# Optimization experiments

Measured on AMD Instinct MI355X. Metric: run time of the kernel, lower is better.

## Reference

```python
import jax, jax.numpy as jnp
import numpy as np
from math import ceil

B, N, C_IN, H, EDIM = 64, 512, 128, 128, 5
EPG = 16 * N          # edges per graph
E = B * EPG           # 524288 edges total
K1 = ceil(0.5 * N)    # 256 clusters after pool 1
K2 = ceil(0.5 * K1)   # 128 clusters after pool 2
EPS = 1e-15


def dense_mincut_pool(x, adj, s, mask=None):
    # x: [B,n,F], adj: [B,n,n], s: [B,n,k]
    s = jax.nn.softmax(s, axis=-1)
    if mask is not None:
        m = mask[..., None].astype(x.dtype)
        x = x * m
        s = s * m
    out = jnp.einsum('bnk,bnf->bkf', s, x)
    out_adj = jnp.einsum('bnk,bnm,bml->bkl', s, adj, s)
    mincut_num = jnp.trace(out_adj, axis1=-2, axis2=-1)
    d_flat = adj.sum(-1)                                   # degrees [B,n]
    mincut_den = jnp.trace(jnp.einsum('bnk,bn,bnl->bkl', s, d_flat, s), axis1=-2, axis2=-1)
    mincut_loss = jnp.mean(-(mincut_num / mincut_den))
    k = s.shape[-1]
    ss = jnp.einsum('bnk,bnl->bkl', s, s)
    ss_norm = jnp.linalg.norm(ss, axis=(-1, -2), keepdims=True)
    i_s = jnp.eye(k, dtype=x.dtype)
    ortho_loss = jnp.mean(jnp.linalg.norm(ss / ss_norm - i_s / np.sqrt(k), axis=(-1, -2)))
    out_adj = out_adj * (1.0 - i_s)                        # zero diagonal
    d = jnp.sqrt(out_adj.sum(-1))[..., None] + EPS
    out_adj = out_adj / d / jnp.swapaxes(d, -1, -2)
    return out, out_adj, mincut_loss, ortho_loss


def setup_inputs() -> dict:
    key = jax.random.key(0)
    ks = iter(jax.random.split(key, 40))
    NT = B * N
    x = jax.random.normal(next(ks), (NT, C_IN), jnp.float32)
    # within-graph random edges; nodes are sorted by graph (batch = repeat)
    offs = jnp.repeat(jnp.arange(B, dtype=jnp.int32) * N, EPG)
    src = jax.random.randint(next(ks), (E,), 0, N, jnp.int32) + offs
    dst = jax.random.randint(next(ks), (E,), 0, N, jnp.int32) + offs
    edge_index = jnp.stack([src, dst])
    edge_attr = jax.random.normal(next(ks), (E, EDIM), jnp.float32)
    batch = jnp.repeat(jnp.arange(B, dtype=jnp.int32), N)

    def W(shape):
        return jax.random.normal(next(ks), shape, jnp.float32) * 0.05

    inp = dict(x=x, edge_index=edge_index, edge_attr=edge_attr, batch=batch,
               bn_gamma=jnp.ones((C_IN,), jnp.float32), bn_beta=jnp.zeros((C_IN,), jnp.float32),
               Wq=W((C_IN, H)), bq=W((H,)), Wk=W((C_IN, H)), bk=W((H,)),
               Wv=W((C_IN, H)), bv=W((H,)), We=W((EDIM, H)),
               Wskip=W((C_IN, H)), bskip=W((H,)),
               W_mlp1=W((H, K1)), b_mlp1=W((K1,)),
               W2_rel=W((H, H)), b2_rel=W((H,)), W2_root=W((H, H)),
               W_mlp2=W((H, K2)), b_mlp2=W((K2,)),
               W3_rel=W((H, H)), b3_rel=W((H,)), W3_root=W((H, H)),
               W_lin1=W((H, H)), b_lin1=W((H,)),
               W_ro=W((H, 1)), b_ro=W((1,)))
    return inp


def reference(x, edge_index, edge_attr, batch, bn_gamma, bn_beta,
              Wq, bq, Wk, bk, Wv, bv, We, Wskip, bskip,
              W_mlp1, b_mlp1, W2_rel, b2_rel, W2_root,
              W_mlp2, b_mlp2, W3_rel, b3_rel, W3_root,
              W_lin1, b_lin1, W_ro, b_ro):
    NT = x.shape[0]
    # BatchNorm1d (training-mode batch statistics, biased var, eps=1e-5)
    mu = x.mean(0)
    var = x.var(0)
    xh = (x - mu) / jnp.sqrt(var + 1e-5) * bn_gamma + bn_beta

    # TransformerConv (heads=1, concat=True, root_weight=True, edge_dim=5)
    src, dst = edge_index[0], edge_index[1]
    q = xh @ Wq + bq
    k_ = xh @ Wk + bk
    v = xh @ Wv + bv
    e = edge_attr @ We                       # lin_edge has no bias
    kj = k_[src] + e
    vj = v[src] + e
    logits = (q[dst] * kj).sum(-1) / np.sqrt(H)
    m = jax.ops.segment_max(logits, dst, num_segments=NT)
    a = jnp.exp(logits - m[dst])
    denom = jax.ops.segment_sum(a, dst, num_segments=NT)
    alpha = a / denom[dst]
    agg = jax.ops.segment_sum(alpha[:, None] * vj, dst, num_segments=NT)
    h = jax.nn.relu(agg + xh @ Wskip + bskip)

    # to_dense_batch: equal-size graphs sorted by batch -> reshape
    xd = h.reshape(B, N, H)
    mask = jnp.ones((B, N), bool)
    # to_dense_adj: scatter-add edge indicators (duplicates accumulate)
    adj = jnp.zeros((B, N, N), jnp.float32).at[batch[src], src % N, dst % N].add(1.0)

    s = xd @ W_mlp1 + b_mlp1
    xd, adj, mc1, o1 = dense_mincut_pool(xd, adj, s, mask)
    # DenseGraphConv: lin_rel(adj @ x) + lin_root(x)
    xd = jax.nn.relu((adj @ xd) @ W2_rel + b2_rel + xd @ W2_root)
    s = xd @ W_mlp2 + b_mlp2
    xd, adj, mc2, o2 = dense_mincut_pool(xd, adj, s)
    xd = (adj @ xd) @ W3_rel + b3_rel + xd @ W3_root
    g = xd.mean(1)
    g = jax.nn.relu(g @ W_lin1 + b_lin1)
    return jax.nn.sigmoid(g @ W_ro + b_ro).squeeze(-1)   # [B]
```

## Files before the change

### kernel.cpp

```cpp
#include <hip/hip_runtime.h>
#include <math.h>

#define BGRAPH 64
#define NNODE  512
#define NTOT   32768
#define CIN    128
#define HDIM   128
#define EDIM_  5
#define EDGES  524288
#define K1C    256
#define K2C    128

using f32x4 = __attribute__((ext_vector_type(4))) float;
using s16x8 = __attribute__((ext_vector_type(8))) short;

__device__ __forceinline__ short f2bf(float f) {
    union { float f; unsigned u; } v; v.f = f;
    unsigned r = v.u + 0x7fffu + ((v.u >> 16) & 1u);
    return (short)(r >> 16);
}
__device__ __forceinline__ float bf2f(short s) {
    union { unsigned u; float f; } v; v.u = ((unsigned)(unsigned short)s) << 16;
    return v.f;
}

__global__ __launch_bounds__(256) void bn_stats_kernel(const float* __restrict__ x,
                                                       float* __restrict__ psum,
                                                       float* __restrict__ psq) {
    int tid = threadIdx.x, bid = blockIdx.x;
    long idx0 = (long)bid * 256 + tid;
    float4 s = {0.f, 0.f, 0.f, 0.f}, q = {0.f, 0.f, 0.f, 0.f};
#pragma unroll
    for (int it = 0; it < 16; ++it) {
        float4 v = *(const float4*)(x + (idx0 + (long)it * 65536) * 4);
        s.x += v.x; s.y += v.y; s.z += v.z; s.w += v.w;
        q.x += v.x * v.x; q.y += v.y * v.y; q.z += v.z * v.z; q.w += v.w * v.w;
    }
    __shared__ float ss[128], sq[128];
    if (tid < 128) { ss[tid] = 0.f; sq[tid] = 0.f; }
    __syncthreads();
    int c0 = (tid & 31) * 4;
    atomicAdd(&ss[c0 + 0], s.x); atomicAdd(&ss[c0 + 1], s.y);
    atomicAdd(&ss[c0 + 2], s.z); atomicAdd(&ss[c0 + 3], s.w);
    atomicAdd(&sq[c0 + 0], q.x); atomicAdd(&sq[c0 + 1], q.y);
    atomicAdd(&sq[c0 + 2], q.z); atomicAdd(&sq[c0 + 3], q.w);
    __syncthreads();
    if (tid < 128) {
        psum[bid * 128 + tid] = ss[tid];
        psq[bid * 128 + tid]  = sq[tid];
    }
}

__global__ __launch_bounds__(128) void bn_finalize_kernel(const float* __restrict__ psum,
                                                          const float* __restrict__ psq,
                                                          const float* __restrict__ gamma,
                                                          const float* __restrict__ beta,
                                                          float* __restrict__ scale,
                                                          float* __restrict__ shift) {
    int c = threadIdx.x;
    float s = 0.f, q = 0.f;
    for (int b = 0; b < 256; ++b) { s += psum[b * 128 + c]; q += psq[b * 128 + c]; }
    float mu  = s / (float)NTOT;
    float var = q / (float)NTOT - mu * mu;
    float rstd = rsqrtf(var + 1e-5f);
    float sc = gamma[c] * rstd;
    scale[c] = sc;
    shift[c] = beta[c] - mu * sc;
}

__global__ __launch_bounds__(256) void pack_hist_kernel(const float* __restrict__ Wq, const float* __restrict__ Wk,
                                                        const float* __restrict__ Wv, const float* __restrict__ Ws,
                                                        const float* __restrict__ bq, const float* __restrict__ bk,
                                                        const float* __restrict__ bv, const float* __restrict__ bs,
                                                        float* __restrict__ W4, float* __restrict__ bias4,
                                                        const int* __restrict__ ei,
                                                        int* __restrict__ deg_src,
                                                        int* __restrict__ deg_dst) {
    int bid = blockIdx.x;
    if (bid < 256) {
        int i = bid * 256 + threadIdx.x;
        if (i < 128 * 512) {
            int k = i / 512, j = i % 512;
            float v;
            if (j < 128)      v = Wq[k * 128 + j];
            else if (j < 256) v = Wk[k * 128 + (j - 128)];
            else if (j < 384) v = Wv[k * 128 + (j - 256)];
            else              v = Ws[k * 128 + (j - 384)];
            W4[i] = v;
        }
        if (i < 512) {
            float v;
            if (i < 128)      v = bq[i];
            else if (i < 256) v = bk[i - 128];
            else if (i < 384) v = bv[i - 256];
            else              v = bs[i - 384];
            bias4[i] = v;
        }
    } else {
        int e = (bid - 256) * 256 + threadIdx.x;
        if (e < EDGES) {
            atomicAdd(&deg_src[ei[e]], 1);
            atomicAdd(&deg_dst[ei[EDGES + e]], 1);
        }
    }
}

__global__ __launch_bounds__(1024) void scan2_kernel(const int* __restrict__ deg_src,
                                                     int* __restrict__ rp_src, int* __restrict__ cur_src,
                                                     const int* __restrict__ deg_dst,
                                                     int* __restrict__ rp_dst, int* __restrict__ cur_dst) {
    const int* deg = blockIdx.x ? deg_dst : deg_src;
    int* rowptr    = blockIdx.x ? rp_dst  : rp_src;
    int* cursor    = blockIdx.x ? cur_dst : cur_src;
    __shared__ int part[1024];
    int tid = threadIdx.x;
    int base = tid * 32;
    int s = 0;
    for (int i = 0; i < 32; ++i) s += deg[base + i];
    part[tid] = s;
    __syncthreads();
    for (int off = 1; off < 1024; off <<= 1) {
        int v = part[tid];
        int add = (tid >= off) ? part[tid - off] : 0;
        __syncthreads();
        part[tid] = v + add;
        __syncthreads();
    }
    int run = (tid == 0) ? 0 : part[tid - 1];
    for (int i = 0; i < 32; ++i) {
        rowptr[base + i] = run;
        cursor[base + i] = run;
        run += deg[base + i];
    }
}

__global__ __launch_bounds__(256) void scatter_kernel(const int* __restrict__ ei,
                                                      int* __restrict__ cur_src, int* __restrict__ cur_dst,
                                                      int* __restrict__ eid_src, int* __restrict__ eid_dst) {
    int e = blockIdx.x * 256 + threadIdx.x;
    if (e < EDGES) {
        int s = ei[e], d = ei[EDGES + e];
        eid_src[atomicAdd(&cur_src[s], 1)] = e;
        eid_dst[atomicAdd(&cur_dst[d], 1)] = e;
    }
}

template <int TILE, bool TRANS_A, bool AFFINE, bool ANORM, bool RELU, bool DUAL,
          bool OBF16, bool AU8, bool BBF16, bool ATRBF16, bool ABF16>
__global__ __launch_bounds__(256) void mgemm(const void* __restrict__ Av,
                                             const void* __restrict__ Bv,
                                             const void* __restrict__ A2v,
                                             const void* __restrict__ B2v,
                                             int Ksplit,
                                             const float* __restrict__ bias,
                                             void* __restrict__ Cv,
                                             const float* __restrict__ scale,
                                             const float* __restrict__ shift,
                                             int M, int Nc, int K,
                                             int lda, int ldb, int ldc,
                                             long sA, long sB, long sC) {
    __shared__ __align__(16) short As[TILE * 40];
    __shared__ __align__(16) short Bs[TILE * 40];
    constexpr int ASZ = AU8 ? 1 : ((ATRBF16 || ABF16) ? 2 : 4);
    constexpr int BSZ = BBF16 ? 2 : 4;
    const char* Abase = (const char*)Av + (long)blockIdx.z * sA * ASZ;
    const char* Bbase = (const char*)Bv + (long)blockIdx.z * sB * BSZ;
    float* C = (float*)Cv + (OBF16 ? 0 : (long)blockIdx.z * sC);
    short* Cs = (short*)Cv + (OBF16 ? (long)blockIdx.z * sC : 0);
    const int m0 = blockIdx.y * TILE, n0 = blockIdx.x * TILE;
    const int tid = threadIdx.x;
    const int lane16 = tid & 15;
    const int quad = (tid & 63) >> 4;
    const int wrow = (tid >> 6) >> 1, wcol = (tid >> 6) & 1;
    constexpr int WT = TILE / 32;

    f32x4 acc[WT][WT] = {};

    for (int k0 = 0; k0 < K; k0 += 32) {
        const char* Au = Abase; const char* Bu = Bbase; int ku = k0;
        if (DUAL && k0 >= Ksplit) { Au = (const char*)A2v; Bu = (const char*)B2v; ku = k0 - Ksplit; }

        if (!TRANS_A) {
#pragma unroll
            for (int p = 0; p < TILE / 32; ++p) {
                int idx = tid + p * 256;
                int row = idx >> 3, c4 = idx & 7;
                short4 o;
                if (AU8) {
                    unsigned u = *(const unsigned*)((const unsigned char*)Au +
                                                    (long)(m0 + row) * lda + ku + c4 * 4);
                    o = make_short4(f2bf((float)(u & 255u)), f2bf((float)((u >> 8) & 255u)),
                                    f2bf((float)((u >> 16) & 255u)), f2bf((float)((u >> 24) & 255u)));
                } else if (ABF16) {
                    o = *(const short4*)((const short*)Au + (long)(m0 + row) * lda + ku + c4 * 4);
                } else {
                    float4 v = *(const float4*)((const float*)Au + (long)(m0 + row) * lda + ku + c4 * 4);
                    if (AFFINE) {
                        int k = ku + c4 * 4;
                        v.x = v.x * scale[k] + shift[k];
                        v.y = v.y * scale[k + 1] + shift[k + 1];
                        v.z = v.z * scale[k + 2] + shift[k + 2];
                        v.w = v.w * scale[k + 3] + shift[k + 3];
                    }
                    if (ANORM) {
                        int k = ku + c4 * 4;
                        int grow = m0 + row;
                        const float* dv = scale + (long)blockIdx.z * lda;
                        float dr = dv[grow];
                        v.x = (grow == k + 0) ? 0.f : v.x * dr * dv[k + 0];
                        v.y = (grow == k + 1) ? 0.f : v.y * dr * dv[k + 1];
                        v.z = (grow == k + 2) ? 0.f : v.z * dr * dv[k + 2];
                        v.w = (grow == k + 3) ? 0.f : v.w * dr * dv[k + 3];
                    }
                    o = make_short4(f2bf(v.x), f2bf(v.y), f2bf(v.z), f2bf(v.w));
                }
                *(short4*)&As[row * 40 + c4 * 4] = o;
            }
        } else {
            if (TILE == 128 || tid < 128) {
                int c4 = tid >> 3, g = tid & 7;
                short* d = &As[(c4 * 4) * 40 + g * 4];
                if (ATRBF16) {
                    const short* src = (const short*)Au + (long)(ku + g * 4) * lda + m0 + c4 * 4;
                    short4 r0 = *(const short4*)(src);
                    short4 r1 = *(const short4*)(src + lda);
                    short4 r2 = *(const short4*)(src + 2 * lda);
                    short4 r3 = *(const short4*)(src + 3 * lda);
                    *(short4*)(d + 0 * 40) = make_short4(r0.x, r1.x, r2.x, r3.x);
                    *(short4*)(d + 1 * 40) = make_short4(r0.y, r1.y, r2.y, r3.y);
                    *(short4*)(d + 2 * 40) = make_short4(r0.z, r1.z, r2.z, r3.z);
                    *(short4*)(d + 3 * 40) = make_short4(r0.w, r1.w, r2.w, r3.w);
                } else {
                    const float* src = (const float*)Au + (long)(ku + g * 4) * lda + m0 + c4 * 4;
                    float4 r0 = *(const float4*)(src);
                    float4 r1 = *(const float4*)(src + lda);
                    float4 r2 = *(const float4*)(src + 2 * lda);
                    float4 r3 = *(const float4*)(src + 3 * lda);
                    *(short4*)(d + 0 * 40) = make_short4(f2bf(r0.x), f2bf(r1.x), f2bf(r2.x), f2bf(r3.x));
                    *(short4*)(d + 1 * 40) = make_short4(f2bf(r0.y), f2bf(r1.y), f2bf(r2.y), f2bf(r3.y));
                    *(short4*)(d + 2 * 40) = make_short4(f2bf(r0.z), f2bf(r1.z), f2bf(r2.z), f2bf(r3.z));
                    *(short4*)(d + 3 * 40) = make_short4(f2bf(r0.w), f2bf(r1.w), f2bf(r2.w), f2bf(r3.w));
                }
            }
        }
        if (TILE == 128 || tid < 128) {
            int c4 = tid >> 3, g = tid & 7;
            short* d = &Bs[(c4 * 4) * 40 + g * 4];
            if (BBF16) {
                const short* src = (const short*)Bu + (long)(ku + g * 4) * ldb + n0 + c4 * 4;
                short4 r0 = *(const short4*)(src);
                short4 r1 = *(const short4*)(src + ldb);
                short4 r2 = *(const short4*)(src + 2 * ldb);
                short4 r3 = *(const short4*)(src + 3 * ldb);
                *(short4*)(d + 0 * 40) = make_short4(r0.x, r1.x, r2.x, r3.x);
                *(short4*)(d + 1 * 40) = make_short4(r0.y, r1.y, r2.y, r3.y);
                *(short4*)(d + 2 * 40) = make_short4(r0.z, r1.z, r2.z, r3.z);
                *(short4*)(d + 3 * 40) = make_short4(r0.w, r1.w, r2.w, r3.w);
            } else {
                const float* src = (const float*)Bu + (long)(ku + g * 4) * ldb + n0 + c4 * 4;
                float4 r0 = *(const float4*)(src);
                float4 r1 = *(const float4*)(src + ldb);
                float4 r2 = *(const float4*)(src + 2 * ldb);
                float4 r3 = *(const float4*)(src + 3 * ldb);
                *(short4*)(d + 0 * 40) = make_short4(f2bf(r0.x), f2bf(r1.x), f2bf(r2.x), f2bf(r3.x));
                *(short4*)(d + 1 * 40) = make_short4(f2bf(r0.y), f2bf(r1.y), f2bf(r2.y), f2bf(r3.y));
                *(short4*)(d + 2 * 40) = make_short4(f2bf(r0.z), f2bf(r1.z), f2bf(r2.z), f2bf(r3.z));
                *(short4*)(d + 3 * 40) = make_short4(f2bf(r0.w), f2bf(r1.w), f2bf(r2.w), f2bf(r3.w));
            }
        }
        __syncthreads();

        s16x8 af[WT], bf[WT];
#pragma unroll
        for (int t = 0; t < WT; ++t) {
            af[t] = *(const s16x8*)&As[(wrow * (TILE / 2) + t * 16 + lane16) * 40 + quad * 8];
            bf[t] = *(const s16x8*)&Bs[(wcol * (TILE / 2) + t * 16 + lane16) * 40 + quad * 8];
        }
#pragma unroll
        for (int i = 0; i < WT; ++i)
#pragma unroll
            for (int j = 0; j < WT; ++j)
                acc[i][j] = __builtin_amdgcn_mfma_f32_16x16x32_bf16(af[i], bf[j], acc[i][j], 0, 0, 0);
        __syncthreads();
    }

#pragma unroll
    for (int i = 0; i < WT; ++i) {
        int gm = m0 + wrow * (TILE / 2) + i * 16 + quad * 4;
#pragma unroll
        for (int j = 0; j < WT; ++j) {
            int gn = n0 + wcol * (TILE / 2) + j * 16 + lane16;
            float bv = bias ? bias[gn] : 0.f;
#pragma unroll
            for (int r = 0; r < 4; ++r) {
                float val = acc[i][j][r] + bv;
                if (RELU) val = fmaxf(val, 0.f);
                if (OBF16) Cs[(long)(gm + r) * ldc + gn] = f2bf(val);
                else       C[(long)(gm + r) * ldc + gn] = val;
            }
        }
    }
}

template <int KADJ, bool RELU, bool OBF16>
__global__ __launch_bounds__(256) void fused_gc_kernel(const float* __restrict__ adj,
                                                       const float* __restrict__ dinv,
                                                       const float* __restrict__ xp,
                                                       const float* __restrict__ Wrel,
                                                       const float* __restrict__ brel,
                                                       const float* __restrict__ Wroot,
                                                       void* __restrict__ Outv) {
    __shared__ __align__(16) short As[64 * 40];
    __shared__ __align__(16) short Bs[128 * 40];
    __shared__ __align__(16) short Tl[64][136];
    const int z = blockIdx.y;
    const int m0 = blockIdx.x * 64;
    const int tid = threadIdx.x;
    const int lane16 = tid & 15;
    const int quad = (tid & 63) >> 4;
    const int wrow = (tid >> 6) >> 1, wcol = (tid >> 6) & 1;
    const float* adjz = adj + (long)z * KADJ * KADJ;
    const float* dv   = dinv + (long)z * KADJ;
    const float* xpz  = xp + (long)z * KADJ * 128;

    f32x4 acc[2][4] = {};
    for (int k0 = 0; k0 < KADJ; k0 += 32) {
#pragma unroll
        for (int p = 0; p < 2; ++p) {
            int idx = tid + p * 256;
            int row = idx >> 3, c4 = idx & 7;
            int grow = m0 + row, k = k0 + c4 * 4;
            float4 v = *(const float4*)(adjz + (long)grow * KADJ + k);
            float dr = dv[grow];
            v.x = (grow == k + 0) ? 0.f : v.x * dr * dv[k + 0];
            v.y = (grow == k + 1) ? 0.f : v.y * dr * dv[k + 1];
            v.z = (grow == k + 2) ? 0.f : v.z * dr * dv[k + 2];
            v.w = (grow == k + 3) ? 0.f : v.w * dr * dv[k + 3];
            *(short4*)&As[row * 40 + c4 * 4] =
                make_short4(f2bf(v.x), f2bf(v.y), f2bf(v.z), f2bf(v.w));
        }
        {
            int c4 = tid >> 3, g = tid & 7;
            short* d = &Bs[(c4 * 4) * 40 + g * 4];
            const float* src = xpz + (long)(k0 + g * 4) * 128 + c4 * 4;
            float4 r0 = *(const float4*)(src);
            float4 r1 = *(const float4*)(src + 128);
            float4 r2 = *(const float4*)(src + 256);
            float4 r3 = *(const float4*)(src + 384);
            *(short4*)(d + 0 * 40) = make_short4(f2bf(r0.x), f2bf(r1.x), f2bf(r2.x), f2bf(r3.x));
            *(short4*)(d + 1 * 40) = make_short4(f2bf(r0.y), f2bf(r1.y), f2bf(r2.y), f2bf(r3.y));
            *(short4*)(d + 2 * 40) = make_short4(f2bf(r0.z), f2bf(r1.z), f2bf(r2.z), f2bf(r3.z));
            *(short4*)(d + 3 * 40) = make_short4(f2bf(r0.w), f2bf(r1.w), f2bf(r2.w), f2bf(r3.w));
        }
        __syncthreads();
        s16x8 af[2], bf[4];
#pragma unroll
        for (int t = 0; t < 2; ++t)
            af[t] = *(const s16x8*)&As[(wrow * 32 + t * 16 + lane16) * 40 + quad * 8];
#pragma unroll
        for (int j = 0; j < 4; ++j)
            bf[j] = *(const s16x8*)&Bs[(wcol * 64 + j * 16 + lane16) * 40 + quad * 8];
#pragma unroll
        for (int t = 0; t < 2; ++t)
#pragma unroll
            for (int j = 0; j < 4; ++j)
                acc[t][j] = __builtin_amdgcn_mfma_f32_16x16x32_bf16(af[t], bf[j], acc[t][j], 0, 0, 0);
        __syncthreads();
    }
#pragma unroll
    for (int t = 0; t < 2; ++t)
#pragma unroll
        for (int j = 0; j < 4; ++j)
#pragma unroll
            for (int r = 0; r < 4; ++r)
                Tl[wrow * 32 + t * 16 + quad * 4 + r][wcol * 64 + j * 16 + lane16] =
                    f2bf(acc[t][j][r]);
    __syncthreads();

    f32x4 acc2[2][4] = {};
    for (int k0 = 0; k0 < 256; k0 += 32) {
        const bool useXp = (k0 >= 128);
        const float* Wsrc = useXp ? (Wroot + (long)(k0 - 128) * 128)
                                  : (Wrel + (long)k0 * 128);
        {
            int c4 = tid >> 3, g = tid & 7;
            short* d = &Bs[(c4 * 4) * 40 + g * 4];
            const float* src = Wsrc + (long)(g * 4) * 128 + c4 * 4;
            float4 r0 = *(const float4*)(src);
            float4 r1 = *(const float4*)(src + 128);
            float4 r2 = *(const float4*)(src + 256);
            float4 r3 = *(const float4*)(src + 384);
            *(short4*)(d + 0 * 40) = make_short4(f2bf(r0.x), f2bf(r1.x), f2bf(r2.x), f2bf(r3.x));
            *(short4*)(d + 1 * 40) = make_short4(f2bf(r0.y), f2bf(r1.y), f2bf(r2.y), f2bf(r3.y));
            *(short4*)(d + 2 * 40) = make_short4(f2bf(r0.z), f2bf(r1.z), f2bf(r2.z), f2bf(r3.z));
            *(short4*)(d + 3 * 40) = make_short4(f2bf(r0.w), f2bf(r1.w), f2bf(r2.w), f2bf(r3.w));
        }
        if (useXp) {
#pragma unroll
            for (int p = 0; p < 2; ++p) {
                int idx = tid + p * 256;
                int row = idx >> 3, c4 = idx & 7;
                float4 v = *(const float4*)(xpz + (long)(m0 + row) * 128 + (k0 - 128) + c4 * 4);
                *(short4*)&As[row * 40 + c4 * 4] =
                    make_short4(f2bf(v.x), f2bf(v.y), f2bf(v.z), f2bf(v.w));
            }
        }
        __syncthreads();
        s16x8 af[2], bf[4];
#pragma unroll
        for (int t = 0; t < 2; ++t) {
            int ar = wrow * 32 + t * 16 + lane16;
            af[t] = useXp ? *(const s16x8*)&As[ar * 40 + quad * 8]
                          : *(const s16x8*)&Tl[ar][k0 + quad * 8];
        }
#pragma unroll
        for (int j = 0; j < 4; ++j)
            bf[j] = *(const s16x8*)&Bs[(wcol * 64 + j * 16 + lane16) * 40 + quad * 8];
#pragma unroll
        for (int t = 0; t < 2; ++t)
#pragma unroll
            for (int j = 0; j < 4; ++j)
                acc2[t][j] = __builtin_amdgcn_mfma_f32_16x16x32_bf16(af[t], bf[j], acc2[t][j], 0, 0, 0);
        __syncthreads();
    }

    float* Of = (float*)Outv;
    short* Ob = (short*)Outv;
#pragma unroll
    for (int t = 0; t < 2; ++t) {
#pragma unroll
        for (int j = 0; j < 4; ++j) {
            int gcol = wcol * 64 + j * 16 + lane16;
            float bv = brel[gcol];
#pragma unroll
            for (int r = 0; r < 4; ++r) {
                int grow = m0 + wrow * 32 + t * 16 + quad * 4 + r;
                float val = acc2[t][j][r] + bv;
                if (RELU) val = fmaxf(val, 0.f);
                long oi = ((long)z * KADJ + grow) * 128 + gcol;
                if (OBF16) Ob[oi] = f2bf(val);
                else       Of[oi] = val;
            }
        }
    }
}

template <int NC>
__global__ __launch_bounds__(256) void mlp_softmax_kernel(const short* __restrict__ A,
                                                          const float* __restrict__ W,
                                                          const float* __restrict__ bias,
                                                          short* __restrict__ Out) {
    __shared__ __align__(16) short As[64 * 40];
    __shared__ __align__(16) short Ws[NC * 40];
    const int tid = threadIdx.x;
    const int lane16 = tid & 15;
    const int quad = (tid & 63) >> 4;
    const int wv = tid >> 6;
    const int m0 = blockIdx.x * 64;
    constexpr int NT = NC / 16;

    f32x4 acc[NT] = {};

    for (int k0 = 0; k0 < 128; k0 += 32) {
        {
            int row = tid >> 2, g = tid & 3;
            *(s16x8*)&As[row * 40 + g * 8] =
                *(const s16x8*)(A + (long)(m0 + row) * 128 + k0 + g * 8);
        }
#pragma unroll
        for (int p = 0; p < NC / 128; ++p) {
            int c4 = tid >> 3, g = tid & 7;
            int n0 = p * 128 + c4 * 4;
            short* d = &Ws[n0 * 40 + g * 4];
            const float* src = W + (long)(k0 + g * 4) * NC + n0;
            float4 r0 = *(const float4*)(src);
            float4 r1 = *(const float4*)(src + NC);
            float4 r2 = *(const float4*)(src + 2 * NC);
            float4 r3 = *(const float4*)(src + 3 * NC);
            *(short4*)(d + 0 * 40) = make_short4(f2bf(r0.x), f2bf(r1.x), f2bf(r2.x), f2bf(r3.x));
            *(short4*)(d + 1 * 40) = make_short4(f2bf(r0.y), f2bf(r1.y), f2bf(r2.y), f2bf(r3.y));
            *(short4*)(d + 2 * 40) = make_short4(f2bf(r0.z), f2bf(r1.z), f2bf(r2.z), f2bf(r3.z));
            *(short4*)(d + 3 * 40) = make_short4(f2bf(r0.w), f2bf(r1.w), f2bf(r2.w), f2bf(r3.w));
        }
        __syncthreads();

        s16x8 af = *(const s16x8*)&As[(wv * 16 + lane16) * 40 + quad * 8];
#pragma unroll
        for (int t = 0; t < NT; ++t) {
            s16x8 bf = *(const s16x8*)&Ws[(t * 16 + lane16) * 40 + quad * 8];
            acc[t] = __builtin_amdgcn_mfma_f32_16x16x32_bf16(af, bf, acc[t], 0, 0, 0);
// ... 144 lines not shown

    float qw[EDIM_];
    {
        s16x8 qv = *(const s16x8*)(qkvs + (long)node * 512 + lane * 8);
        float qf[8];
#pragma unroll
        for (int j = 0; j < 8; ++j) qf[j] = bf2f(qv[j]);
#pragma unroll
        for (int d = 0; d < EDIM_; ++d) {
            float p = 0.f;
#pragma unroll
            for (int j = 0; j < 8; ++j) p += qf[j] * sWe[d * 128 + lane * 8 + j];
            qw[d] = p;
        }
#pragma unroll
        for (int off = 8; off; off >>= 1)
#pragma unroll
            for (int d = 0; d < EDIM_; ++d) qw[d] += __shfl_xor(qw[d], off);
#pragma unroll
        for (int d = 0; d < EDIM_; ++d) qw[d] *= 0.08838834764831845f;
    }

    int start = rp_dst[node], cnt = deg_dst[node];
    int nch = (cnt + 15) >> 4;

    float lsum = 0.f, a5[EDIM_] = {};
    int   src_c[4] = {0, 0, 0, 0};
    float a_c[4]   = {0.f, 0.f, 0.f, 0.f};
    for (int c = 0; c < nch; ++c) {
        int t = c * 16 + lane;
        int src = 0; float wv = 0.f;
        if (t < cnt) {
            int e = eid_dst[start + t];
            src = ei[e];
            float lg = bf2f(Sl[src & 511]);
            float ea[EDIM_];
#pragma unroll
            for (int d = 0; d < EDIM_; ++d) { ea[d] = eattr[e * EDIM_ + d]; lg += ea[d] * qw[d]; }
            wv = expf(lg);
            lsum += wv;
#pragma unroll
            for (int d = 0; d < EDIM_; ++d) a5[d] += wv * ea[d];
        }
        if (c < 4) { src_c[c] = src; a_c[c] = wv; }
        else if (t < cnt) alpha[start + t] = wv;
    }
#pragma unroll
    for (int off = 8; off; off >>= 1) {
        lsum += __shfl_xor(lsum, off);
#pragma unroll
        for (int d = 0; d < EDIM_; ++d) a5[d] += __shfl_xor(a5[d], off);
    }
    float inv = (lsum > 0.f) ? 1.f / lsum : 0.f;
    float e5[EDIM_];
#pragma unroll
    for (int d = 0; d < EDIM_; ++d) e5[d] = a5[d] * inv;

    float acc[8] = {};
    for (int c = 0; c < nch; ++c) {
        int src; float a;
        if (c < 4) { src = src_c[c]; a = a_c[c]; }
        else {
            int t = c * 16 + lane;
            if (t < cnt) {
                int e = eid_dst[start + t];
                src = ei[e];
                a = alpha[start + t];
            } else { src = 0; a = 0.f; }
        }
        int m = min(16, cnt - c * 16);
        if (m == 16) {
#pragma unroll
            for (int j = 0; j < 16; ++j) {
                int   sj = __shfl(src, gbase + j);
                float aj = __shfl(a,   gbase + j);
                s16x8 v = *(const s16x8*)(qkvs + (long)sj * 512 + 256 + lane * 8);
#pragma unroll
                for (int k = 0; k < 8; ++k) acc[k] += aj * bf2f(v[k]);
            }
        } else {
            for (int j = 0; j < m; ++j) {
                int   sj = __shfl(src, gbase + j);
                float aj = __shfl(a,   gbase + j);
                s16x8 v = *(const s16x8*)(qkvs + (long)sj * 512 + 256 + lane * 8);
#pragma unroll
                for (int k = 0; k < 8; ++k) acc[k] += aj * bf2f(v[k]);
            }
        }
    }

    s16x8 sk = *(const s16x8*)(qkvs + (long)node * 512 + 384 + lane * 8);
    s16x8 o;
#pragma unroll
    for (int j = 0; j < 8; ++j) {
        float ec = 0.f;
#pragma unroll
        for (int d = 0; d < EDIM_; ++d) ec += e5[d] * sWe[d * 128 + lane * 8 + j];
        float val = acc[j] * inv + ec + bf2f(sk[j]);
        o[j] = f2bf(fmaxf(val, 0.f));
    }
    *(s16x8*)(h + (long)node * 128 + lane * 8) = o;
}

__global__ __launch_bounds__(256) void t1_gather_kernel(const int* __restrict__ ei,
                                                        const int* __restrict__ rp_src,
                                                        const int* __restrict__ deg_src,
                                                        const int* __restrict__ eid_src,
                                                        const short* __restrict__ s1b,
                                                        short* __restrict__ T1s) {
    int g = threadIdx.x >> 4;
    int lane = threadIdx.x & 15;
    int gbase = (threadIdx.x & 63) & ~15;
    int b = blockIdx.x;
    int xcd = b & 7, idx = b >> 3;
    int nb = (xcd * 8 + (idx >> 5)) * 32 + (idx & 31);
    int node = nb * 16 + g;

    int start = rp_src[node], cnt = deg_src[node];
    int nch = (cnt + 15) >> 4;
    float acc[16] = {};
    for (int c = 0; c < nch; ++c) {
        int t = c * 16 + lane;
        int dst = 0;
        if (t < cnt) {
            int e = eid_src[start + t];
            dst = ei[EDGES + e];
        }
        int m = min(16, cnt - c * 16);
        if (m == 16) {
#pragma unroll
            for (int j = 0; j < 16; ++j) {
                int dj = __shfl(dst, gbase + j);
                const s16x8* p = (const s16x8*)(s1b + (long)dj * 256 + lane * 16);
                s16x8 v0 = p[0], v1 = p[1];
#pragma unroll
                for (int k = 0; k < 8; ++k) { acc[k] += bf2f(v0[k]); acc[8 + k] += bf2f(v1[k]); }
            }
        } else {
            for (int j = 0; j < m; ++j) {
                int dj = __shfl(dst, gbase + j);
                const s16x8* p = (const s16x8*)(s1b + (long)dj * 256 + lane * 16);
                s16x8 v0 = p[0], v1 = p[1];
#pragma unroll
                for (int k = 0; k < 8; ++k) { acc[k] += bf2f(v0[k]); acc[8 + k] += bf2f(v1[k]); }
            }
        }
    }
    s16x8 o0, o1;
#pragma unroll
    for (int k = 0; k < 8; ++k) { o0[k] = f2bf(acc[k]); o1[k] = f2bf(acc[8 + k]); }
    short* o = T1s + (long)node * 256 + lane * 16;
    *(s16x8*)(o)     = o0;
    *(s16x8*)(o + 8) = o1;
}

template <int KC>
__global__ __launch_bounds__(256) void dinv_kernel(const float* __restrict__ adj,
                                                   float* __restrict__ dinv) {
    int wave = threadIdx.x >> 6;
    int lane = threadIdx.x & 63;
    int row = blockIdx.x * 4 + wave;
    int b = row / KC, r = row % KC;
    const float* p = adj + (long)b * KC * KC + (long)r * KC;
    float s = 0.f;
    for (int j = lane; j < KC; j += 64)
        if (j != r) s += p[j];
#pragma unroll
    for (int off = 32; off; off >>= 1) s += __shfl_xor(s, off);
    if (lane == 0) dinv[row] = 1.f / (sqrtf(s) + 1e-15f);
}

__global__ __launch_bounds__(128) void readout_kernel(const float* __restrict__ xd3,
                                                      const float* __restrict__ W_lin1,
                                                      const float* __restrict__ b_lin1,
                                                      const float* __restrict__ W_ro,
                                                      const float* __restrict__ b_ro,
                                                      float* __restrict__ out) {
    int b = blockIdx.x, t = threadIdx.x;
    __shared__ float g[128], g2[128], wred[2];
    const float* X = xd3 + (long)b * K2C * 128;
    float s = 0.f;
    for (int r = 0; r < K2C; ++r) s += X[r * 128 + t];
    g[t] = s * (1.f / (float)K2C);
    __syncthreads();
    float u = b_lin1[t];
    for (int k = 0; k < 128; ++k) u += g[k] * W_lin1[k * 128 + t];
    g2[t] = fmaxf(u, 0.f);
    __syncthreads();
    float p = g2[t] * W_ro[t];
#pragma unroll
    for (int off = 32; off; off >>= 1) p += __shfl_xor(p, off);
    if ((t & 63) == 0) wred[t >> 6] = p;
    __syncthreads();
    if (t == 0) {
        float tot = wred[0] + wred[1] + b_ro[0];
        out[b] = 1.f / (1.f + expf(-tot));
    }
}

extern "C" void kernel_launch(void* const* d_in, const int* in_sizes, int n_in,
                              void* d_out, int out_size, void* d_ws, size_t ws_size,
                              hipStream_t stream) {
    const float* x      = (const float*)d_in[0];
    const int*   ei     = (const int*)d_in[1];
    const float* eattr  = (const float*)d_in[2];
    const float* gamma  = (const float*)d_in[4];
    const float* beta   = (const float*)d_in[5];
    const float* Wq     = (const float*)d_in[6];
    const float* bq     = (const float*)d_in[7];
    const float* Wk     = (const float*)d_in[8];
    const float* bk     = (const float*)d_in[9];
    const float* Wv     = (const float*)d_in[10];
    const float* bv     = (const float*)d_in[11];
    const float* We     = (const float*)d_in[12];
    const float* Wskip  = (const float*)d_in[13];
    const float* bskip  = (const float*)d_in[14];
    const float* W_mlp1 = (const float*)d_in[15];
    const float* b_mlp1 = (const float*)d_in[16];
    const float* W2_rel = (const float*)d_in[17];
    const float* b2_rel = (const float*)d_in[18];
    const float* W2_root= (const float*)d_in[19];
    const float* W_mlp2 = (const float*)d_in[20];
    const float* b_mlp2 = (const float*)d_in[21];
    const float* W3_rel = (const float*)d_in[22];
    const float* b3_rel = (const float*)d_in[23];
    const float* W3_root= (const float*)d_in[24];
    const float* W_lin1 = (const float*)d_in[25];
    const float* b_lin1 = (const float*)d_in[26];
    const float* W_ro   = (const float*)d_in[27];
    const float* b_ro   = (const float*)d_in[28];
    float* out = (float*)d_out;

    char* w = (char*)d_ws;
    const size_t MB = 1ull << 20;
    short* qkvs = (short*)(w + 0);
    short* S    = (short*)(w + 32 * MB);
    short* T1s  = (short*)(w + 48 * MB);
    short* s1b  = (short*)(w + 64 * MB);
    short* xd2  = (short*)(w + 56 * MB);
    short* s2b  = (short*)(w + 72 * MB);
    float* t2   = (float*)(w + 64 * MB);
    float* adj2 = (float*)(w + 0);
    float* xp2  = (float*)(w + 4 * MB);
    float* xd3  = (float*)(w + 12 * MB);
    short* h    = (short*)(w + 80 * MB);
    float* adj1 = (float*)(w + 80 * MB);
    float* xp1  = (float*)(w + 96 * MB);
    float* alpha= (float*)(w + 97 * MB);
    char* misc  = w + 104 * MB;
    float* W4     = (float*)(misc + 0x00000);
    float* bias4  = (float*)(misc + 0x40000);
    float* scale  = (float*)(misc + 0x41400);
    float* shift  = (float*)(misc + 0x41600);
    float* dinv1  = (float*)(misc + 0x42000);
    float* dinv2  = (float*)(misc + 0x52000);
    int* deg_src  = (int*)(misc + 0x60000);
    int* deg_dst  = (int*)(misc + 0x80000);
    int* rp_src   = (int*)(misc + 0xA0000);
    int* rp_dst   = (int*)(misc + 0xC0000);
    int* cur_src  = (int*)(misc + 0xE0000);
    int* cur_dst  = (int*)(misc + 0x100000);
    int* eid_src  = (int*)(misc + 0x120000);
    int* eid_dst  = (int*)(misc + 0x320000);
    float* psum   = (float*)(misc + 0x520000);
    float* psq    = (float*)(misc + 0x540000);

    hipMemsetAsync(deg_src, 0, 2 * NTOT * sizeof(int), stream);

    bn_stats_kernel<<<256, 256, 0, stream>>>(x, psum, psq);
    bn_finalize_kernel<<<1, 128, 0, stream>>>(psum, psq, gamma, beta, scale, shift);

    pack_hist_kernel<<<2304, 256, 0, stream>>>(Wq, Wk, Wv, Wskip, bq, bk, bv, bskip,
                                               W4, bias4, ei, deg_src, deg_dst);

    scan2_kernel<<<2, 1024, 0, stream>>>(deg_src, rp_src, cur_src, deg_dst, rp_dst, cur_dst);
    scatter_kernel<<<EDGES / 256, 256, 0, stream>>>(ei, cur_src, cur_dst, eid_src, eid_dst);

    mgemm<128, false, true, false, false, false, true, false, false, false, false>
        <<<dim3(4, 256, 1), 256, 0, stream>>>(
        x, W4, nullptr, nullptr, 0, bias4, qkvs, scale, shift,
        NTOT, 512, 128, 128, 512, 512, 0, 0, 0);

    bgemm<true><<<dim3(4, 4, BGRAPH), 256, 0, stream>>>(
        qkvs + 0, qkvs + 128, S, 0.08838834764831845f,
        NNODE, NNODE, 128, 512, 512, 512,
        (long)NNODE * 512, (long)NNODE * 512, (long)NNODE * NNODE);

    attn_pv_kernel<<<NTOT / 16, 256, 0, stream>>>(
        S, ei, eattr, We, rp_dst, deg_dst, eid_dst, qkvs, alpha, h);

    mlp_softmax_kernel<K1C><<<NTOT / 64, 256, 0, stream>>>(h, W_mlp1, b_mlp1, s1b);

    t1_gather_kernel<<<NTOT / 16, 256, 0, stream>>>(
        ei, rp_src, deg_src, eid_src, s1b, T1s);

    mgemm<64, true, false, false, false, false, false, false, true, true, false>
        <<<dim3(2, 4, BGRAPH), 256, 0, stream>>>(
        s1b, h, nullptr, nullptr, 0, nullptr, xp1, nullptr, nullptr,
        K1C, 128, NNODE, K1C, 128, 128,
        (long)NNODE * K1C, (long)NNODE * 128, (long)K1C * 128);
    mgemm<128, true, false, false, false, false, false, false, true, true, false>
        <<<dim3(2, 2, BGRAPH), 256, 0, stream>>>(
        s1b, T1s, nullptr, nullptr, 0, nullptr, adj1, nullptr, nullptr,
        K1C, K1C, NNODE, K1C, K1C, K1C,
        (long)NNODE * K1C, (long)NNODE * K1C, (long)K1C * K1C);

    dinv_kernel<K1C><<<(BGRAPH * K1C) / 4, 256, 0, stream>>>(adj1, dinv1);

    fused_gc_kernel<K1C, true, true><<<dim3(4, BGRAPH), 256, 0, stream>>>(
        adj1, dinv1, xp1, W2_rel, b2_rel, W2_root, xd2);

    mlp_softmax_kernel<K2C><<<(BGRAPH * K1C) / 64, 256, 0, stream>>>(xd2, W_mlp2, b_mlp2, s2b);

    mgemm<64, false, false, true, false, false, false, false, true, false, false>
        <<<dim3(2, 4, BGRAPH), 256, 0, stream>>>(
        adj1, s2b, nullptr, nullptr, 0, nullptr, t2, dinv1, nullptr,
        K1C, K2C, K1C, K1C, K2C, K2C,
        (long)K1C * K1C, (long)K1C * K2C, (long)K1C * K2C);
    mgemm<64, true, false, false, false, false, false, false, false, true, false>
        <<<dim3(2, 2, BGRAPH), 256, 0, stream>>>(
        s2b, t2, nullptr, nullptr, 0, nullptr, adj2, nullptr, nullptr,
        K2C, K2C, K1C, K2C, K2C, K2C,
        (long)K1C * K2C, (long)K1C * K2C, (long)K2C * K2C);
    mgemm<64, true, false, false, false, false, false, false, true, true, false>
        <<<dim3(2, 2, BGRAPH), 256, 0, stream>>>(
        s2b, xd2, nullptr, nullptr, 0, nullptr, xp2, nullptr, nullptr,
        K2C, 128, K1C, K2C, 128, 128,
        (long)K1C * K2C, (long)K1C * 128, (long)K2C * 128);

    dinv_kernel<K2C><<<(BGRAPH * K2C) / 4, 256, 0, stream>>>(adj2, dinv2);

    fused_gc_kernel<K2C, false, false><<<dim3(2, BGRAPH), 256, 0, stream>>>(
        adj2, dinv2, xp2, W3_rel, b3_rel, W3_root, xd3);

    readout_kernel<<<BGRAPH, 128, 0, stream>>>(xd3, W_lin1, b_lin1, W_ro, b_ro, out);

    (void)in_sizes; (void)n_in; (void)out_size; (void)ws_size;
}
```

Before: 498.1 us.

## Fuse prep kernels and compute adjacency row sums in GEMM epilogue

Merges the BN stats, weight packing and degree histogram into one prep kernel, and folds the BN finalize into the scan launch as an extra block. The separate dinv kernels are removed: the adjacency GEMMs now accumulate off-diagonal row sums via atomics in their epilogue, and consumers compute the inverse sqrt degree into shared memory. This cuts launches and the extra pass over the adjacency matrices, at the cost of float atomics (nondeterministic summation order) and a larger memset.

```diff
diff --git a/kernel.cpp b/kernel.cpp
--- a/kernel.cpp
+++ b/kernel.cpp
@@ -24,61 +24,42 @@
     return v.f;
 }
 
-__global__ __launch_bounds__(256) void bn_stats_kernel(const float* __restrict__ x,
-                                                       float* __restrict__ psum,
-                                                       float* __restrict__ psq) {
+__global__ __launch_bounds__(256) void prep_kernel(const float* __restrict__ x,
+                                                   float* __restrict__ psum,
+                                                   float* __restrict__ psq,
+                                                   const float* __restrict__ Wq, const float* __restrict__ Wk,
+                                                   const float* __restrict__ Wv, const float* __restrict__ Ws,
+                                                   const float* __restrict__ bq, const float* __restrict__ bk,
+                                                   const float* __restrict__ bv, const float* __restrict__ bs,
+                                                   float* __restrict__ W4, float* __restrict__ bias4,
+                                                   const int* __restrict__ ei,
+                                                   int* __restrict__ deg_src,
+                                                   int* __restrict__ deg_dst) {
+    __shared__ float ss[128], sq[128];
     int tid = threadIdx.x, bid = blockIdx.x;
-    long idx0 = (long)bid * 256 + tid;
-    float4 s = {0.f, 0.f, 0.f, 0.f}, q = {0.f, 0.f, 0.f, 0.f};
-#pragma unroll
-    for (int it = 0; it < 16; ++it) {
-        float4 v = *(const float4*)(x + (idx0 + (long)it * 65536) * 4);
-        s.x += v.x; s.y += v.y; s.z += v.z; s.w += v.w;
-        q.x += v.x * v.x; q.y += v.y * v.y; q.z += v.z * v.z; q.w += v.w * v.w;
-    }
-    __shared__ float ss[128], sq[128];
-    if (tid < 128) { ss[tid] = 0.f; sq[tid] = 0.f; }
-    __syncthreads();
-    int c0 = (tid & 31) * 4;
-    atomicAdd(&ss[c0 + 0], s.x); atomicAdd(&ss[c0 + 1], s.y);
-    atomicAdd(&ss[c0 + 2], s.z); atomicAdd(&ss[c0 + 3], s.w);
-    atomicAdd(&sq[c0 + 0], q.x); atomicAdd(&sq[c0 + 1], q.y);
-    atomicAdd(&sq[c0 + 2], q.z); atomicAdd(&sq[c0 + 3], q.w);
-    __syncthreads();
-    if (tid < 128) {
-        psum[bid * 128 + tid] = ss[tid];
-        psq[bid * 128 + tid]  = sq[tid];
-    }
-}
-
-__global__ __launch_bounds__(128) void bn_finalize_kernel(const float* __restrict__ psum,
-                                                          const float* __restrict__ psq,
-                                                          const float* __restrict__ gamma,
-                                                          const float* __restrict__ beta,
-                                                          float* __restrict__ scale,
-                                                          float* __restrict__ shift) {
-    int c = threadIdx.x;
-    float s = 0.f, q = 0.f;
-    for (int b = 0; b < 256; ++b) { s += psum[b * 128 + c]; q += psq[b * 128 + c]; }
-    float mu  = s / (float)NTOT;
-    float var = q / (float)NTOT - mu * mu;
-    float rstd = rsqrtf(var + 1e-5f);
-    float sc = gamma[c] * rstd;
-    scale[c] = sc;
-    shift[c] = beta[c] - mu * sc;
-}
-
-__global__ __launch_bounds__(256) void pack_hist_kernel(const float* __restrict__ Wq, const float* __restrict__ Wk,
-                                                        const float* __restrict__ Wv, const float* __restrict__ Ws,
-                                                        const float* __restrict__ bq, const float* __restrict__ bk,
-                                                        const float* __restrict__ bv, const float* __restrict__ bs,
-                                                        float* __restrict__ W4, float* __restrict__ bias4,
-                                                        const int* __restrict__ ei,
-                                                        int* __restrict__ deg_src,
-                                                        int* __restrict__ deg_dst) {
-    int bid = blockIdx.x;
     if (bid < 256) {
-        int i = bid * 256 + threadIdx.x;
+        long idx0 = (long)bid * 256 + tid;
+        float4 s = {0.f, 0.f, 0.f, 0.f}, q = {0.f, 0.f, 0.f, 0.f};
+#pragma unroll
+        for (int it = 0; it < 16; ++it) {
+            float4 v = *(const float4*)(x + (idx0 + (long)it * 65536) * 4);
+            s.x += v.x; s.y += v.y; s.z += v.z; s.w += v.w;
+            q.x += v.x * v.x; q.y += v.y * v.y; q.z += v.z * v.z; q.w += v.w * v.w;
+        }
+        if (tid < 128) { ss[tid] = 0.f; sq[tid] = 0.f; }
+        __syncthreads();
+        int c0 = (tid & 31) * 4;
+        atomicAdd(&ss[c0 + 0], s.x); atomicAdd(&ss[c0 + 1], s.y);
+        atomicAdd(&ss[c0 + 2], s.z); atomicAdd(&ss[c0 + 3], s.w);
+        atomicAdd(&sq[c0 + 0], q.x); atomicAdd(&sq[c0 + 1], q.y);
+        atomicAdd(&sq[c0 + 2], q.z); atomicAdd(&sq[c0 + 3], q.w);
+        __syncthreads();
+        if (tid < 128) {
+            psum[bid * 128 + tid] = ss[tid];
+            psq[bid * 128 + tid]  = sq[tid];
+        }
+    } else if (bid < 512) {
+        int i = (bid - 256) * 256 + tid;
         if (i < 128 * 512) {
             int k = i / 512, j = i % 512;
             float v;
@@ -97,7 +78,7 @@
             bias4[i] = v;
         }
     } else {
-        int e = (bid - 256) * 256 + threadIdx.x;
+        int e = (bid - 512) * 256 + tid;
         if (e < EDGES) {
             atomicAdd(&deg_src[ei[e]], 1);
             atomicAdd(&deg_dst[ei[EDGES + e]], 1);
@@ -105,15 +86,35 @@
     }
 }
 
-__global__ __launch_bounds__(1024) void scan2_kernel(const int* __restrict__ deg_src,
-                                                     int* __restrict__ rp_src, int* __restrict__ cur_src,
-                                                     const int* __restrict__ deg_dst,
-                                                     int* __restrict__ rp_dst, int* __restrict__ cur_dst) {
+__global__ __launch_bounds__(1024) void scan2fin_kernel(const int* __restrict__ deg_src,
+                                                        int* __restrict__ rp_src, int* __restrict__ cur_src,
+                                                        const int* __restrict__ deg_dst,
+                                                        int* __restrict__ rp_dst, int* __restrict__ cur_dst,
+                                                        const float* __restrict__ psum,
+                                                        const float* __restrict__ psq,
+                                                        const float* __restrict__ gamma,
+                                                        const float* __restrict__ beta,
+                                                        float* __restrict__ scale,
+                                                        float* __restrict__ shift) {
+    __shared__ int part[1024];
+    int tid = threadIdx.x;
+    if (blockIdx.x == 2) {
+        if (tid < 128) {
+            int c = tid;
+            float s = 0.f, q = 0.f;
+            for (int b = 0; b < 256; ++b) { s += psum[b * 128 + c]; q += psq[b * 128 + c]; }
+            float mu  = s / (float)NTOT;
+            float var = q / (float)NTOT - mu * mu;
+            float rstd = rsqrtf(var + 1e-5f);
+            float sc = gamma[c] * rstd;
+            scale[c] = sc;
+            shift[c] = beta[c] - mu * sc;
+        }
+        return;
+    }
     const int* deg = blockIdx.x ? deg_dst : deg_src;
     int* rowptr    = blockIdx.x ? rp_dst  : rp_src;
     int* cursor    = blockIdx.x ? cur_dst : cur_src;
-    __shared__ int part[1024];
-    int tid = threadIdx.x;
     int base = tid * 32;
     int s = 0;
     for (int i = 0; i < 32; ++i) s += deg[base + i];
@@ -145,8 +146,8 @@
     }
 }
 
-template <int TILE, bool TRANS_A, bool AFFINE, bool ANORM, bool RELU, bool DUAL,
-          bool OBF16, bool AU8, bool BBF16, bool ATRBF16, bool ABF16>
+template <int TILE, bool TRANS_A, bool AFFINE, bool ANORM, bool ROWSUM, bool RELU,
+          bool DUAL, bool OBF16, bool AU8, bool BBF16, bool ATRBF16, bool ABF16>
 __global__ __launch_bounds__(256) void mgemm(const void* __restrict__ Av,
                                              const void* __restrict__ Bv,
                                              const void* __restrict__ A2v,
@@ -161,6 +162,7 @@
                                              long sA, long sB, long sC) {
     __shared__ __align__(16) short As[TILE * 40];
     __shared__ __align__(16) short Bs[TILE * 40];
+    __shared__ float dvl[ANORM ? 256 : 1];
     constexpr int ASZ = AU8 ? 1 : ((ATRBF16 || ABF16) ? 2 : 4);
     constexpr int BSZ = BBF16 ? 2 : 4;
     const char* Abase = (const char*)Av + (long)blockIdx.z * sA * ASZ;
@@ -173,6 +175,12 @@
     const int quad = (tid & 63) >> 4;
     const int wrow = (tid >> 6) >> 1, wcol = (tid >> 6) & 1;
     constexpr int WT = TILE / 32;
+
+    if (ANORM) {
+        for (int i = tid; i < K; i += 256)
+            dvl[i] = 1.f / (sqrtf(scale[(long)blockIdx.z * lda + i]) + 1e-15f);
+        __syncthreads();
+    }
 
     f32x4 acc[WT][WT] = {};
 
@@ -205,12 +213,11 @@
                     if (ANORM) {
                         int k = ku + c4 * 4;
                         int grow = m0 + row;
-                        const float* dv = scale + (long)blockIdx.z * lda;
-                        float dr = dv[grow];
-                        v.x = (grow == k + 0) ? 0.f : v.x * dr * dv[k + 0];
-                        v.y = (grow == k + 1) ? 0.f : v.y * dr * dv[k + 1];
-                        v.z = (grow == k + 2) ? 0.f : v.z * dr * dv[k + 2];
-                        v.w = (grow == k + 3) ? 0.f : v.w * dr * dv[k + 3];
+                        float dr = dvl[grow];
+                        v.x = (grow == k + 0) ? 0.f : v.x * dr * dvl[k + 0];
+                        v.y = (grow == k + 1) ? 0.f : v.y * dr * dvl[k + 1];
+                        v.z = (grow == k + 2) ? 0.f : v.z * dr * dvl[k + 2];
+                        v.w = (grow == k + 3) ? 0.f : v.w * dr * dvl[k + 3];
                     }
                     o = make_short4(f2bf(v.x), f2bf(v.y), f2bf(v.z), f2bf(v.w));
                 }
@@ -300,11 +307,39 @@
             }
         }
     }
+
+    if (ROWSUM) {
+        float* rlA = (float*)As;
+        float* rlB = (float*)Bs;
+#pragma unroll
+        for (int i = 0; i < WT; ++i) {
+#pragma unroll
+            for (int r = 0; r < 4; ++r) {
+                int gm = m0 + wrow * (TILE / 2) + i * 16 + quad * 4 + r;
+                float p = 0.f;
+#pragma unroll
+                for (int j = 0; j < WT; ++j) {
+                    int gn = n0 + wcol * (TILE / 2) + j * 16 + lane16;
+                    p += (gn == gm) ? 0.f : acc[i][j][r];
+                }
+#pragma unroll
+                for (int off = 1; off < 16; off <<= 1) p += __shfl_xor(p, off);
+                if (lane16 == 0) {
+                    int rl = wrow * (TILE / 2) + i * 16 + quad * 4 + r;
+                    (wcol ? rlB : rlA)[rl] = p;
+                }
+            }
+        }
+        __syncthreads();
+        float* rout = (float*)shift;
+        for (int t = tid; t < TILE; t += 256)
+            atomicAdd(&rout[(long)blockIdx.z * M + m0 + t], rlA[t] + rlB[t]);
+    }
 }
 
 template <int KADJ, bool RELU, bool OBF16>
 __global__ __launch_bounds__(256) void fused_gc_kernel(const float* __restrict__ adj,
-                                                       const float* __restrict__ dinv,
+                                                       const float* __restrict__ rowsum,
                                                        const float* __restrict__ xp,
                                                        const float* __restrict__ Wrel,
                                                        const float* __restrict__ brel,
@@ -313,6 +348,7 @@
     __shared__ __align__(16) short As[64 * 40];
     __shared__ __align__(16) short Bs[128 * 40];
     __shared__ __align__(16) short Tl[64][136];
+    __shared__ float dvl[KADJ];
     const int z = blockIdx.y;
     const int m0 = blockIdx.x * 64;
     const int tid = threadIdx.x;
@@ -320,8 +356,11 @@
     const int quad = (tid & 63) >> 4;
     const int wrow = (tid >> 6) >> 1, wcol = (tid >> 6) & 1;
     const float* adjz = adj + (long)z * KADJ * KADJ;
-    const float* dv   = dinv + (long)z * KADJ;
     const float* xpz  = xp + (long)z * KADJ * 128;
+
+    for (int i = tid; i < KADJ; i += 256)
+        dvl[i] = 1.f / (sqrtf(rowsum[(long)z * KADJ + i]) + 1e-15f);
+    __syncthreads();
 
     f32x4 acc[2][4] = {};
     for (int k0 = 0; k0 < KADJ; k0 += 32) {
@@ -331,11 +370,11 @@
             int row = idx >> 3, c4 = idx & 7;
             int grow = m0 + row, k = k0 + c4 * 4;
             float4 v = *(const float4*)(adjz + (long)grow * KADJ + k);
-            float dr = dv[grow];
-            v.x = (grow == k + 0) ? 0.f : v.x * dr * dv[k + 0];
-            v.y = (grow == k + 1) ? 0.f : v.y * dr * dv[k + 1];
-            v.z = (grow == k + 2) ? 0.f : v.z * dr * dv[k + 2];
-            v.w = (grow == k + 3) ? 0.f : v.w * dr * dv[k + 3];
+            float dr = dvl[grow];
+            v.x = (grow == k + 0) ? 0.f : v.x * dr * dvl[k + 0];
+            v.y = (grow == k + 1) ? 0.f : v.y * dr * dvl[k + 1];
+            v.z = (grow == k + 2) ? 0.f : v.z * dr * dvl[k + 2];
+            v.w = (grow == k + 3) ? 0.f : v.w * dr * dvl[k + 3];
             *(short4*)&As[row * 40 + c4 * 4] =
                 make_short4(f2bf(v.x), f2bf(v.y), f2bf(v.z), f2bf(v.w));
         }
@@ -786,22 +825,6 @@
     short* o = T1s + (long)node * 256 + lane * 16;
     *(s16x8*)(o)     = o0;
     *(s16x8*)(o + 8) = o1;
-}
-
-template <int KC>
-__global__ __launch_bounds__(256) void dinv_kernel(const float* __restrict__ adj,
-                                                   float* __restrict__ dinv) {
-    int wave = threadIdx.x >> 6;
-    int lane = threadIdx.x & 63;
-    int row = blockIdx.x * 4 + wave;
-    int b = row / KC, r = row % KC;
-    const float* p = adj + (long)b * KC * KC + (long)r * KC;
-    float s = 0.f;
-    for (int j = lane; j < KC; j += 64)
-        if (j != r) s += p[j];
-#pragma unroll
-    for (int off = 32; off; off >>= 1) s += __shfl_xor(s, off);
-    if (lane == 0) dinv[row] = 1.f / (sqrtf(s) + 1e-15f);
 }
 
 __global__ __launch_bounds__(128) void readout_kernel(const float* __restrict__ xd3,
@@ -886,8 +909,8 @@
     float* bias4  = (float*)(misc + 0x40000);
     float* scale  = (float*)(misc + 0x41400);
     float* shift  = (float*)(misc + 0x41600);
-    float* dinv1  = (float*)(misc + 0x42000);
-    float* dinv2  = (float*)(misc + 0x52000);
+    float* rowsum1= (float*)(misc + 0x42000);
+    float* rowsum2= (float*)(misc + 0x52000);
     int* deg_src  = (int*)(misc + 0x60000);
     int* deg_dst  = (int*)(misc + 0x80000);
     int* rp_src   = (int*)(misc + 0xA0000);
@@ -899,18 +922,19 @@
     float* psum   = (float*)(misc + 0x520000);
     float* psq    = (float*)(misc + 0x540000);
 
-    hipMemsetAsync(deg_src, 0, 2 * NTOT * sizeof(int), stream);
-
-    bn_stats_kernel<<<256, 256, 0, stream>>>(x, psum, psq);
-    bn_finalize_kernel<<<1, 128, 0, stream>>>(psum, psq, gamma, beta, scale, shift);
-
-    pack_hist_kernel<<<2304, 256, 0, stream>>>(Wq, Wk, Wv, Wskip, bq, bk, bv, bskip,
-                                               W4, bias4, ei, deg_src, deg_dst);
-
-    scan2_kernel<<<2, 1024, 0, stream>>>(deg_src, rp_src, cur_src, deg_dst, rp_dst, cur_dst);
+    hipMemsetAsync(misc + 0x42000, 0, 0xA0000 - 0x42000, stream);
+
+    prep_kernel<<<2560, 256, 0, stream>>>(x, psum, psq,
+                                          Wq, Wk, Wv, Wskip, bq, bk, bv, bskip,
+                                          W4, bias4, ei, deg_src, deg_dst);
+
+    scan2fin_kernel<<<3, 1024, 0, stream>>>(deg_src, rp_src, cur_src,
+                                            deg_dst, rp_dst, cur_dst,
+                                            psum, psq, gamma, beta, scale, shift);
+
     scatter_kernel<<<EDGES / 256, 256, 0, stream>>>(ei, cur_src, cur_dst, eid_src, eid_dst);
 
-    mgemm<128, false, true, false, false, false, true, false, false, false, false>
+    mgemm<128, false, true, false, false, false, false, true, false, false, false, false>
         <<<dim3(4, 256, 1), 256, 0, stream>>>(
         x, W4, nullptr, nullptr, 0, bias4, qkvs, scale, shift,
         NTOT, 512, 128, 128, 512, 512, 0, 0, 0);
@@ -928,44 +952,40 @@
     t1_gather_kernel<<<NTOT / 16, 256, 0, stream>>>(
         ei, rp_src, deg_src, eid_src, s1b, T1s);
 
-    mgemm<64, true, false, false, false, false, false, false, true, true, false>
+    mgemm<64, true, false, false, false, false, false, false, false, true, true, false>
         <<<dim3(2, 4, BGRAPH), 256, 0, stream>>>(
         s1b, h, nullptr, nullptr, 0, nullptr, xp1, nullptr, nullptr,
         K1C, 128, NNODE, K1C, 128, 128,
         (long)NNODE * K1C, (long)NNODE * 128, (long)K1C * 128);
-    mgemm<128, true, false, false, false, false, false, false, true, true, false>
+    mgemm<128, true, false, false, true, false, false, false, false, true, true, false>
         <<<dim3(2, 2, BGRAPH), 256, 0, stream>>>(
-        s1b, T1s, nullptr, nullptr, 0, nullptr, adj1, nullptr, nullptr,
+        s1b, T1s, nullptr, nullptr, 0, nullptr, adj1, nullptr, rowsum1,
         K1C, K1C, NNODE, K1C, K1C, K1C,
         (long)NNODE * K1C, (long)NNODE * K1C, (long)K1C * K1C);
 
-    dinv_kernel<K1C><<<(BGRAPH * K1C) / 4, 256, 0, stream>>>(adj1, dinv1);
-
     fused_gc_kernel<K1C, true, true><<<dim3(4, BGRAPH), 256, 0, stream>>>(
-        adj1, dinv1, xp1, W2_rel, b2_rel, W2_root, xd2);
+        adj1, rowsum1, xp1, W2_rel, b2_rel, W2_root, xd2);
 
     mlp_softmax_kernel<K2C><<<(BGRAPH * K1C) / 64, 256, 0, stream>>>(xd2, W_mlp2, b_mlp2, s2b);
 
-    mgemm<64, false, false, true, false, false, false, false, true, false, false>
+    mgemm<64, false, false, true, false, false, false, false, false, true, false, false>
         <<<dim3(2, 4, BGRAPH), 256, 0, stream>>>(
-        adj1, s2b, nullptr, nullptr, 0, nullptr, t2, dinv1, nullptr,
+        adj1, s2b, nullptr, nullptr, 0, nullptr, t2, rowsum1, nullptr,
         K1C, K2C, K1C, K1C, K2C, K2C,
         (long)K1C * K1C, (long)K1C * K2C, (long)K1C * K2C);
-    mgemm<64, true, false, false, false, false, false, false, false, true, false>
+    mgemm<64, true, false, false, true, false, false, false, false, false, true, false>
         <<<dim3(2, 2, BGRAPH), 256, 0, stream>>>(
-        s2b, t2, nullptr, nullptr, 0, nullptr, adj2, nullptr, nullptr,
+        s2b, t2, nullptr, nullptr, 0, nullptr, adj2, nullptr, rowsum2,
         K2C, K2C, K1C, K2C, K2C, K2C,
         (long)K1C * K2C, (long)K1C * K2C, (long)K2C * K2C);
-    mgemm<64, true, false, false, false, false, false, false, true, true, false>
+    mgemm<64, true, false, false, false, false, false, false, false, true, true, false>
         <<<dim3(2, 2, BGRAPH), 256, 0, stream>>>(
         s2b, xd2, nullptr, nullptr, 0, nullptr, xp2, nullptr, nullptr,
         K2C, 128, K1C, K2C, 128, 128,
         (long)K1C * K2C, (long)K1C * 128, (long)K2C * 128);
 
-    dinv_kernel<K2C><<<(BGRAPH * K2C) / 4, 256, 0, stream>>>(adj2, dinv2);
-
     fused_gc_kernel<K2C, false, false><<<dim3(2, BGRAPH), 256, 0, stream>>>(
-        adj2, dinv2, xp2, W3_rel, b3_rel, W3_root, xd3);
+        adj2, rowsum2, xp2, W3_rel, b3_rel, W3_root, xd3);
 
     readout_kernel<<<BGRAPH, 128, 0, stream>>>(xd3, W_lin1, b_lin1, W_ro, b_ro, out);
 
```

Result: faster. 482.2 us (-3.2%).
